# Optimization experiments

Measured on AMD Instinct MI355X. Metric: run time of the kernel, lower is better.

The kernel has to match this reference:

```python
import jax, jax.numpy as jnp
import numpy as np

EPS = 1e-8  # torch.nn.CosineSimilarity default eps


def setup_inputs() -> dict:
    key = jax.random.key(0)
    k1, k2, k3 = jax.random.split(key, 3)
    B, T, D, L = 16, 256, 512, 32
    v1 = jax.random.normal(k1, (B, T, D), dtype=jnp.float32)
    v1_mask = jnp.ones((B, T), dtype=jnp.float32)
    v2 = jax.random.normal(k2, (B, D), dtype=jnp.float32)
    w = jax.random.normal(k3, (L, D), dtype=jnp.float32)
    return {"v1": v1, "v1_mask": v1_mask, "v2": v2, "w": w}


def reference(v1, v1_mask, v2, w):
    # v1: [B,T,D], v1_mask: [B,T], v2: [B,D], w: [L,D]
    # Original math: cos over D of (w * v1) and (w * v2), per perspective l.
    # Fused: (w_l*a)\cdot(w_l*b) = sum_d w[l,d]^2 a[d] b[d]; likewise for norms.
    v1m = v1 * v1_mask[:, :, None]              # [B,T,D]
    w2 = w * w                                   # [L,D]
    num = jnp.einsum('btd,ld,bd->btl', v1m, w2, v2)          # [B,T,L]
    n1 = jnp.sqrt(jnp.einsum('btd,ld->btl', v1m * v1m, w2))  # [B,T,L]
    n2 = jnp.sqrt(jnp.einsum('bd,ld->bl', v2 * v2, w2))      # [B,L]
    denom = jnp.maximum(n1 * n2[:, None, :], EPS)
    return num / denom                           # [B,T,L]
```

## Files before the change

kernel.cpp:

```cpp
#include <hip/hip_runtime.h>
#include <cstddef>

#define EPSV 1e-8f

__device__ __forceinline__ float rdlane(float x, int s) {
    return __int_as_float(__builtin_amdgcn_readlane(__float_as_int(x), s));
}

#define GLD16(gp, lp) \
    __builtin_amdgcn_global_load_lds((const __attribute__((address_space(1))) void*)(gp), \
                                     (__attribute__((address_space(3))) void*)(lp), 16, 0, 0)

__global__ __launch_bounds__(256, 1) void fullmatch_kernel(
    const float* __restrict__ v1,
    const float* __restrict__ v1_mask,
    const float* __restrict__ v2,
    const float* __restrict__ w,
    float* __restrict__ out)
{
    const int tid  = threadIdx.x;
    const int lane = tid & 63;
    const int wv   = tid >> 6;

    const int bid   = blockIdx.x;
    const int xcd   = bid & 7;
    const int slot  = bid >> 3;
    const int tileg = xcd * 8 + (slot >> 2);
    const int lg    = slot & 3;
    const int b  = tileg >> 2;
    const int tc = tileg & 3;
    const int t0 = tc * 64;
    const int p  = lg * 4 + wv;
    const int t  = t0 + lane;

    __shared__ float v1s[2][64][128];

    const size_t v1base = (size_t)(b * 256 + t0) * 512;

    #pragma unroll
    for (int j = 0; j < 8; ++j) {
        const int r0 = (wv * 8 + j) * 2;
        const int r  = r0 + (lane >> 5);
        const int c4 = (lane & 31) ^ (r & 31);
        GLD16(v1 + v1base + (size_t)r * 512 + c4 * 4, &v1s[0][r0][0]);
    }

    float4 w2A[2], w2B[2], hA[2], hB[2];
    float n2pA = 0.f, n2pB = 0.f;
    {
        const float* __restrict__ v2b = v2 + (size_t)b * 512;
        const float* __restrict__ wAp = w + (size_t)p * 512;
        const float* __restrict__ wBp = w + (size_t)(p + 16) * 512;
        #pragma unroll
        for (int q = 0; q < 2; ++q) {
            const int k4 = q * 64 + lane;
            const float4 wa = *(const float4*)(wAp + k4 * 4);
            const float4 wb = *(const float4*)(wBp + k4 * 4);
            const float4 vv = *(const float4*)(v2b + k4 * 4);
            float4 sa, sb, ha, hb;
            sa.x = wa.x*wa.x; sa.y = wa.y*wa.y; sa.z = wa.z*wa.z; sa.w = wa.w*wa.w;
            sb.x = wb.x*wb.x; sb.y = wb.y*wb.y; sb.z = wb.z*wb.z; sb.w = wb.w*wb.w;
            ha.x = sa.x*vv.x; ha.y = sa.y*vv.y; ha.z = sa.z*vv.z; ha.w = sa.w*vv.w;
            hb.x = sb.x*vv.x; hb.y = sb.y*vv.y; hb.z = sb.z*vv.z; hb.w = sb.w*vv.w;
            w2A[q] = sa; w2B[q] = sb; hA[q] = ha; hB[q] = hb;
            n2pA += ha.x*vv.x + ha.y*vv.y + ha.z*vv.z + ha.w*vv.w;
            n2pB += hb.x*vv.x + hb.y*vv.y + hb.z*vv.z + hb.w*vv.w;
        }
    }
    #pragma unroll
    for (int m = 32; m >= 1; m >>= 1) {
        n2pA += __shfl_xor(n2pA, m, 64);
        n2pB += __shfl_xor(n2pB, m, 64);
    }
    const float n2vA = sqrtf(n2pA);
    const float n2vB = sqrtf(n2pB);
    const float mk   = v1_mask[b * 256 + t];

    float accNA = 0.f, accNB = 0.f, accDA = 0.f, accDB = 0.f;

    #pragma unroll
    for (int c = 0; c < 4; ++c) {
        __syncthreads();
        if (c < 3) {
            #pragma unroll
            for (int j = 0; j < 8; ++j) {
                const int r0 = (wv * 8 + j) * 2;
                const int r  = r0 + (lane >> 5);
                const int c4 = (lane & 31) ^ (r & 31);
                GLD16(v1 + v1base + (size_t)r * 512 + (c + 1) * 128 + c4 * 4,
                      &v1s[(c + 1) & 1][r0][0]);
            }
        }
        const float* __restrict__ row = &v1s[c & 1][lane][0];
        const int lm = lane & 31;
        #pragma unroll 8
        for (int s = 0; s < 32; ++s) {
            const float4 a = *(const float4*)(row + ((s ^ lm) << 2));
            const int li = ((c & 1) << 5) + s;
            const float wax = rdlane(w2A[c >> 1].x, li);
            const float way = rdlane(w2A[c >> 1].y, li);
            const float waz = rdlane(w2A[c >> 1].z, li);
            const float waw = rdlane(w2A[c >> 1].w, li);
            const float wbx = rdlane(w2B[c >> 1].x, li);
            const float wby = rdlane(w2B[c >> 1].y, li);
            const float wbz = rdlane(w2B[c >> 1].z, li);
            const float wbw = rdlane(w2B[c >> 1].w, li);
            const float hax = rdlane(hA[c >> 1].x, li);
            const float hay = rdlane(hA[c >> 1].y, li);
            const float haz = rdlane(hA[c >> 1].z, li);
            const float haw = rdlane(hA[c >> 1].w, li);
            const float hbx = rdlane(hB[c >> 1].x, li);
            const float hby = rdlane(hB[c >> 1].y, li);
            const float hbz = rdlane(hB[c >> 1].z, li);
            const float hbw = rdlane(hB[c >> 1].w, li);

            const float x2 = a.x * a.x, y2 = a.y * a.y;
            const float z2 = a.z * a.z, q2 = a.w * a.w;

            accNA = fmaf(a.x, hax, accNA);
            accNA = fmaf(a.y, hay, accNA);
            accNA = fmaf(a.z, haz, accNA);
            accNA = fmaf(a.w, haw, accNA);
            accNB = fmaf(a.x, hbx, accNB);
            accNB = fmaf(a.y, hby, accNB);
            accNB = fmaf(a.z, hbz, accNB);
            accNB = fmaf(a.w, hbw, accNB);
            accDA = fmaf(x2, wax, accDA);
            accDA = fmaf(y2, way, accDA);
            accDA = fmaf(z2, waz, accDA);
            accDA = fmaf(q2, waw, accDA);
            accDB = fmaf(x2, wbx, accDB);
            accDB = fmaf(y2, wby, accDB);
            accDB = fmaf(z2, wbz, accDB);
            accDB = fmaf(q2, wbw, accDB);
        }
    }

    const float amk  = fabsf(mk);
    const float denA = fmaxf(sqrtf(accDA) * amk * n2vA, EPSV);
    const float denB = fmaxf(sqrtf(accDB) * amk * n2vB, EPSV);
    const size_t o = (size_t)(b * 256 + t) * 32;
    out[o + p]      = (accNA * mk) / denA;
    out[o + p + 16] = (accNB * mk) / denB;
}

extern "C" void kernel_launch(void* const* d_in, const int* in_sizes, int n_in,
                              void* d_out, int out_size, void* d_ws, size_t ws_size,
                              hipStream_t stream) {
    const float* v1      = (const float*)d_in[0];
    const float* v1_mask = (const float*)d_in[1];
    const float* v2      = (const float*)d_in[2];
    const float* w       = (const float*)d_in[3];
    float* out           = (float*)d_out;

    fullmatch_kernel<<<dim3(256), dim3(256), 0, stream>>>(v1, v1_mask, v2, w, out);
}
```

Measured before the change: 21.25 us.

## Split D-reduction across wave pairs and double grid to 512 blocks

Each block now handles two perspectives per wave pair instead of four, with pairs of waves splitting each 128-wide D chunk in half and combining partial sums through shared memory before writing. The grid doubles to 512 blocks with launch bounds raised to allow two blocks per CU, and the XCD-aware block remapping is dropped. The aim is more parallelism and shorter per-wave serial reduction loops. The cost is that each v1 tile is now loaded by twice as many blocks, plus an extra barrier and an LDS combine step.

```diff
diff --git a/kernel.cpp b/kernel.cpp
--- a/kernel.cpp
+++ b/kernel.cpp
@@ -11,7 +11,7 @@
     __builtin_amdgcn_global_load_lds((const __attribute__((address_space(1))) void*)(gp), \
                                      (__attribute__((address_space(3))) void*)(lp), 16, 0, 0)
 
-__global__ __launch_bounds__(256, 1) void fullmatch_kernel(
+__global__ __launch_bounds__(256, 2) void fullmatch_kernel(
     const float* __restrict__ v1,
     const float* __restrict__ v1_mask,
     const float* __restrict__ v2,
@@ -21,25 +21,26 @@
     const int tid  = threadIdx.x;
     const int lane = tid & 63;
     const int wv   = tid >> 6;
+    const int lp2  = wv & 1;
+    const int dh   = wv >> 1;
+    const int dh16 = __builtin_amdgcn_readfirstlane(dh) * 16;
 
-    const int bid   = blockIdx.x;
-    const int xcd   = bid & 7;
-    const int slot  = bid >> 3;
-    const int tileg = xcd * 8 + (slot >> 2);
-    const int lg    = slot & 3;
-    const int b  = tileg >> 2;
-    const int tc = tileg & 3;
-    const int t0 = tc * 64;
-    const int p  = lg * 4 + wv;
-    const int t  = t0 + lane;
+    const int bid  = blockIdx.x;
+    const int tile = bid & 63;
+    const int lpg  = bid >> 6;
+    const int b    = tile >> 2;
+    const int t0   = (tile & 3) * 64;
+    const int p    = lpg * 2 + lp2;
+    const int t    = t0 + lane;
 
     __shared__ float v1s[2][64][128];
+    __shared__ float cmb[4][64][4];
 
     const size_t v1base = (size_t)(b * 256 + t0) * 512;
 
     #pragma unroll
     for (int j = 0; j < 8; ++j) {
-        const int r0 = (wv * 8 + j) * 2;
+        const int r0 = wv * 16 + j * 2;
         const int r  = r0 + (lane >> 5);
         const int c4 = (lane & 31) ^ (r & 31);
         GLD16(v1 + v1base + (size_t)r * 512 + c4 * 4, &v1s[0][r0][0]);
@@ -72,11 +73,9 @@
         n2pA += __shfl_xor(n2pA, m, 64);
         n2pB += __shfl_xor(n2pB, m, 64);
     }
-    const float n2vA = sqrtf(n2pA);
-    const float n2vB = sqrtf(n2pB);
-    const float mk   = v1_mask[b * 256 + t];
 
     float accNA = 0.f, accNB = 0.f, accDA = 0.f, accDB = 0.f;
+    const int lm = lane & 31;
 
     #pragma unroll
     for (int c = 0; c < 4; ++c) {
@@ -84,7 +83,7 @@
         if (c < 3) {
             #pragma unroll
             for (int j = 0; j < 8; ++j) {
-                const int r0 = (wv * 8 + j) * 2;
+                const int r0 = wv * 16 + j * 2;
                 const int r  = r0 + (lane >> 5);
                 const int c4 = (lane & 31) ^ (r & 31);
                 GLD16(v1 + v1base + (size_t)r * 512 + (c + 1) * 128 + c4 * 4,
@@ -92,27 +91,29 @@
             }
         }
         const float* __restrict__ row = &v1s[c & 1][lane][0];
-        const int lm = lane & 31;
-        #pragma unroll 8
-        for (int s = 0; s < 32; ++s) {
+        #pragma unroll
+        for (int j = 0; j < 16; ++j) {
+            const int s  = dh16 + j;
             const float4 a = *(const float4*)(row + ((s ^ lm) << 2));
             const int li = ((c & 1) << 5) + s;
-            const float wax = rdlane(w2A[c >> 1].x, li);
-            const float way = rdlane(w2A[c >> 1].y, li);
-            const float waz = rdlane(w2A[c >> 1].z, li);
-            const float waw = rdlane(w2A[c >> 1].w, li);
-            const float wbx = rdlane(w2B[c >> 1].x, li);
-            const float wby = rdlane(w2B[c >> 1].y, li);
-            const float wbz = rdlane(w2B[c >> 1].z, li);
-            const float wbw = rdlane(w2B[c >> 1].w, li);
-            const float hax = rdlane(hA[c >> 1].x, li);
-            const float hay = rdlane(hA[c >> 1].y, li);
-            const float haz = rdlane(hA[c >> 1].z, li);
-            const float haw = rdlane(hA[c >> 1].w, li);
-            const float hbx = rdlane(hB[c >> 1].x, li);
-            const float hby = rdlane(hB[c >> 1].y, li);
-            const float hbz = rdlane(hB[c >> 1].z, li);
-            const float hbw = rdlane(hB[c >> 1].w, li);
+            const int q  = c >> 1;
+
+            const float wax = rdlane(w2A[q].x, li);
+            const float way = rdlane(w2A[q].y, li);
+            const float waz = rdlane(w2A[q].z, li);
+            const float waw = rdlane(w2A[q].w, li);
+            const float wbx = rdlane(w2B[q].x, li);
+            const float wby = rdlane(w2B[q].y, li);
+            const float wbz = rdlane(w2B[q].z, li);
+            const float wbw = rdlane(w2B[q].w, li);
+            const float hax = rdlane(hA[q].x, li);
+            const float hay = rdlane(hA[q].y, li);
+            const float haz = rdlane(hA[q].z, li);
+            const float haw = rdlane(hA[q].w, li);
+            const float hbx = rdlane(hB[q].x, li);
+            const float hby = rdlane(hB[q].y, li);
+            const float hbz = rdlane(hB[q].z, li);
+            const float hbw = rdlane(hB[q].w, li);
 
             const float x2 = a.x * a.x, y2 = a.y * a.y;
             const float z2 = a.z * a.z, q2 = a.w * a.w;
@@ -136,12 +137,29 @@
         }
     }
 
-    const float amk  = fabsf(mk);
-    const float denA = fmaxf(sqrtf(accDA) * amk * n2vA, EPSV);
-    const float denB = fmaxf(sqrtf(accDB) * amk * n2vB, EPSV);
-    const size_t o = (size_t)(b * 256 + t) * 32;
-    out[o + p]      = (accNA * mk) / denA;
-    out[o + p + 16] = (accNB * mk) / denB;
+    cmb[wv][lane][0] = accNA;
+    cmb[wv][lane][1] = accNB;
+    cmb[wv][lane][2] = accDA;
+    cmb[wv][lane][3] = accDB;
+    __syncthreads();
+
+    if (wv < 2) {
+        const float4 o = *(const float4*)(&cmb[wv + 2][lane][0]);
+        const float nA = accNA + o.x;
+        const float nB = accNB + o.y;
+        const float dA = accDA + o.z;
+        const float dB = accDB + o.w;
+
+        const float mk  = v1_mask[b * 256 + t];
+        const float amk = fabsf(mk);
+        const float n2vA = sqrtf(n2pA);
+        const float n2vB = sqrtf(n2pB);
+        const float denA = fmaxf(sqrtf(dA) * amk * n2vA, EPSV);
+        const float denB = fmaxf(sqrtf(dB) * amk * n2vB, EPSV);
+        const size_t oix = (size_t)(b * 256 + t) * 32;
+        out[oix + p]      = (nA * mk) / denA;
+        out[oix + p + 16] = (nB * mk) / denB;
+    }
 }
 
 extern "C" void kernel_launch(void* const* d_in, const int* in_sizes, int n_in,
@@ -153,5 +171,5 @@
     const float* w       = (const float*)d_in[3];
     float* out           = (float*)d_out;
 
-    fullmatch_kernel<<<dim3(256), dim3(256), 0, stream>>>(v1, v1_mask, v2, w, out);
+    fullmatch_kernel<<<dim3(512), dim3(256), 0, stream>>>(v1, v1_mask, v2, w, out);
 }
```

Measured after the change: 19.66 us. 7.5% less time.
